# Performance work log

Measured on AMD Instinct MI355X. Metric: run time of the kernel, lower is better.

Reference implementation:

```python
import jax, jax.numpy as jnp
import numpy as np

BS, V, S, K = 4, 2048, 7, 10
CLASS_NUM, VEC_NUM, CAT = 6, 8, 16
OUT_HEAD = CLASS_NUM + VEC_NUM * 3  # 30
DIM_FUSE = 128 + 128 + 256 + 256 + 512 + 512 + 16  # 1808


def _normalize(x, axis):
    return x / jnp.maximum(jnp.linalg.norm(x, axis=axis, keepdims=True), 1e-12)


def knn_index(verts, k):
    # verts: (b, v, 3) -> (b, v, k) excluding self
    inner = jnp.einsum('bnd,bmd->bnm', verts, verts)
    sq = jnp.sum(verts * verts, axis=2)
    dist = sq[:, :, None] + sq[:, None, :] - 2.0 * inner
    _, idx = jax.lax.top_k(-dist, k + 1)
    return idx[:, :, 1:]


def nearest_index(target, source):
    # target: (b, v1, 3), source: (b, v2, 3) -> (b, v1)
    inner = jnp.einsum('bnd,bmd->bnm', target, source)
    d = jnp.sum(source * source, 2)[:, None, :] + jnp.sum(target * target, 2)[:, :, None] - 2.0 * inner
    return jnp.argmin(d, axis=-1)


def gather_nb(t, idx):
    # t: (b, v, d), idx: (b, v1, k) -> (b, v1, k, d)
    return jax.vmap(lambda tt, ii: tt[ii])(t, idx)


def gather1(t, idx):
    # t: (b, v, d), idx: (b, v1) -> (b, v1, d)
    return jax.vmap(lambda tt, ii: tt[ii])(t, idx)


def bn_train(x, g, b, eps=1e-5):
    # x: (b, v, c); BatchNorm1d training-mode over (batch, vertices)
    m = jnp.mean(x, axis=(0, 1), keepdims=True)
    v = jnp.var(x, axis=(0, 1), keepdims=True)
    return (x - m) * jax.lax.rsqrt(v + eps) * g + b


def conv_surface(nb_idx, verts, directions, s, kernel_num):
    nd = _normalize(gather_nb(verts, nb_idx) - verts[:, :, None, :], -1)  # (b,v,n,3)
    sd = _normalize(directions, 0)  # (3, s*k)
    theta = jax.nn.relu(jnp.einsum('bvnd,dk->bvnk', nd, sd))
    b_, v_, n_, _ = theta.shape
    theta = theta.reshape(b_, v_, n_, s, kernel_num)
    return jnp.sum(jnp.max(theta, axis=2), axis=2)  # (b, v, kernel_num)


def conv_layer(nb_idx, verts, fm, w, b, directions, s, out_ch):
    nd = _normalize(gather_nb(verts, nb_idx) - verts[:, :, None, :], -1)
    sd = _normalize(directions, 0)  # (3, s*out_ch)
    theta = jax.nn.relu(jnp.einsum('bvnd,dk->bvnk', nd, sd))  # (b,v,n,s*o)
    fo = jnp.einsum('bvc,ck->bvk', fm, w) + b  # (b, v, (s+1)*o)
    center = fo[..., :out_ch]
    supp = gather_nb(fo[..., out_ch:], nb_idx)  # (b,v,n,s*o)
    act = (theta * supp).reshape(theta.shape[0], theta.shape[1], theta.shape[2], s, out_ch)
    act = jnp.sum(jnp.max(act, axis=2), axis=2)  # (b, v, o)
    return center + act


def pool_layer(verts, fm, pooling_rate, nb_num):
    idx = knn_index(verts, nb_num)
    pooled = jnp.max(gather_nb(fm, idx), axis=2)
    pool_num = verts.shape[1] // pooling_rate
    # deterministic subsample (torch uses randperm; fixed arange for reproducibility)
    return verts[:, :pool_num], pooled[:, :pool_num]


def setup_inputs() -> dict:
    key = jax.random.key(0)
    ks = jax.random.split(key, 16)
    def rn(i, shape, scale=0.05):
        return jax.random.normal(ks[i], shape, dtype=jnp.float32) * scale
    z = lambda *s: jnp.zeros(s, jnp.float32)
    o = lambda *s: jnp.ones(s, jnp.float32)
    return {
        'vertices': jax.random.normal(ks[0], (BS, V, 3), dtype=jnp.float32),
        'onehot': jax.nn.one_hot(jax.random.randint(ks[1], (BS,), 0, CAT), CAT, dtype=jnp.float32),
        'dir0': rn(2, (3, S * 128)),
        'w1': rn(3, (128, (S + 1) * 128)), 'b1': z((S + 1) * 128), 'dir1': rn(4, (3, S * 128)),
        'w2': rn(5, (128, (S + 1) * 256)), 'b2': z((S + 1) * 256), 'dir2': rn(6, (3, S * 256)),
        'w3': rn(7, (256, (S + 1) * 256)), 'b3': z((S + 1) * 256), 'dir3': rn(8, (3, S * 256)),
        'w4': rn(9, (256, (S + 1) * 512)), 'b4': z((S + 1) * 512), 'dir4': rn(10, (3, S * 512)),
        'g_bn1': o(128), 'be_bn1': z(128),
        'g_bn2': o(256), 'be_bn2': z(256),
        'g_bn3': o(256), 'be_bn3': z(256),
        'wc1': rn(11, (512, DIM_FUSE)), 'bc1': z(512),
        'wc2': rn(12, (512, 512)), 'bc2': z(512),
        'wc3': rn(13, (OUT_HEAD, 512)), 'bc3': z(OUT_HEAD),
    }


def reference(vertices, onehot, dir0, w1, b1, dir1, w2, b2, dir2, w3, b3, dir3,
              w4, b4, dir4, g_bn1, be_bn1, g_bn2, be_bn2, g_bn3, be_bn3,
              wc1, bc1, wc2, bc2, wc3, bc3):
    bs, v_num, _ = vertices.shape
    nb = knn_index(vertices, K)
    fm0 = jax.nn.relu(conv_surface(nb, vertices, dir0, S, 128))
    fm1 = jax.nn.relu(bn_train(conv_layer(nb, vertices, fm0, w1, b1, dir1, S, 128), g_bn1, be_bn1))
    vp1, fp1 = pool_layer(vertices, fm1, 4, 4)
    nb1 = knn_index(vp1, min(K, vp1.shape[1] // 8))
    fm2 = jax.nn.relu(bn_train(conv_layer(nb1, vp1, fp1, w2, b2, dir2, S, 256), g_bn2, be_bn2))
    fm3 = jax.nn.relu(bn_train(conv_layer(nb1, vp1, fm2, w3, b3, dir3, S, 256), g_bn3, be_bn3))
    vp2, fp2 = pool_layer(vp1, fm3, 4, 4)
    nb2 = knn_index(vp2, min(K, vp2.shape[1] // 8))
    fm4 = conv_layer(nb2, vp2, fp2, w4, b4, dir4, S, 512)
    f_global = jnp.max(fm4, axis=1)  # (b, 512)
    n1 = nearest_index(vertices, vp1)
    n2 = nearest_index(vertices, vp2)
    fm2u = gather1(fm2, n1)
    fm3u = gather1(fm3, n1)
    fm4u = gather1(fm4, n2)
    fg = jnp.broadcast_to(f_global[:, None, :], (bs, v_num, 512))
    oh = jnp.broadcast_to(onehot[:, None, :], (bs, v_num, CAT))
    feat = jnp.concatenate([fm0, fm1, fm2u, fm3u, fm4u, oh], axis=2)
    fuse = jnp.concatenate([fm0, fm1, fm2u, fm3u, fm4u, fg, oh], axis=2)
    h = jax.nn.relu(jnp.einsum('bvc,oc->bvo', fuse, wc1) + bc1)
    h = jax.nn.relu(jnp.einsum('bvc,oc->bvo', h, wc2) + bc2)
    pred = jnp.einsum('bvc,oc->bvo', h, wc3) + bc3
    seg = pred[..., :CLASS_NUM]
    vecs = pred[..., CLASS_NUM:CLASS_NUM + VEC_NUM * 3]
    return (seg, vecs, feat)
```

## Files before the change

### kernel.cpp

```cpp
#include <hip/hip_runtime.h>
#include <hip/hip_bf16.h>
#include <math.h>

#define BSZ 4
#define VN 2048
#define SS 7
#define KNB 10

typedef __attribute__((ext_vector_type(8))) short short8;
typedef __attribute__((ext_vector_type(4))) float f32x4;

__device__ inline ushort f2bf(float x) {
    __hip_bfloat16 h = __float2bfloat16(x);
    return *(ushort*)&h;
}

__device__ inline unsigned fenc(float f) {
    unsigned b = __float_as_uint(f);
    return (b & 0x80000000u) ? ~b : (b | 0x80000000u);
}
__device__ inline float fdec(unsigned e) {
    unsigned b = (e & 0x80000000u) ? (e & 0x7FFFFFFFu) : ~e;
    return __uint_as_float(b);
}

#define PB0 8960L
#define PB1 24320L
#define PB2 958208L
#define PB3 1220352L

__global__ void prep_uber(const float* __restrict__ d0, const float* __restrict__ d1,
                          const float* __restrict__ d2, const float* __restrict__ d3,
                          const float* __restrict__ d4,
                          float* __restrict__ s0, float* __restrict__ s1,
                          float* __restrict__ s2, float* __restrict__ s3, float* __restrict__ s4,
                          const float* __restrict__ wc3, float* __restrict__ wc3t,
                          const float* __restrict__ wc1, ushort* __restrict__ wc1b,
                          const float* __restrict__ wc2, ushort* __restrict__ wc2b) {
    long i = blockIdx.x * 256L + threadIdx.x;
    if (i < PB0) {
        const float* src; float* dst; int C, c;
        if (i < 896)        { src = d0; dst = s0; C = 896;  c = (int)i; }
        else if (i < 1792)  { src = d1; dst = s1; C = 896;  c = (int)i - 896; }
        else if (i < 3584)  { src = d2; dst = s2; C = 1792; c = (int)i - 1792; }
        else if (i < 5376)  { src = d3; dst = s3; C = 1792; c = (int)i - 3584; }
        else                { src = d4; dst = s4; C = 3584; c = (int)i - 5376; }
        float a = src[c], b = src[C + c], e = src[2 * C + c];
        float den = fmaxf(sqrtf(a * a + b * b + e * e), 1e-12f);
        dst[c] = a / den; dst[C + c] = b / den; dst[2 * C + c] = e / den;
    } else if (i < PB1) {
        long j = i - PB0;
        int o = (int)(j / 512), k = (int)(j % 512);
        wc3t[(long)k * 30 + o] = wc3[j];
    } else if (i < PB2) {
        long j = i - PB1;
        int c = (int)(j % 1824);
        long r = j / 1824;
        wc1b[j] = f2bf(c < 1808 ? wc1[r * 1808 + c] : 0.f);
    } else if (i < PB3) {
        long j = i - PB2;
        wc2b[j] = f2bf(wc2[j]);
    }
}

__global__ __launch_bounds__(256) void wt_trans_all(const float* __restrict__ w1, const float* __restrict__ w2,
                                                    const float* __restrict__ w3, const float* __restrict__ w4,
                                                    ushort* __restrict__ o1, ushort* __restrict__ o2,
                                                    ushort* __restrict__ o3, ushort* __restrict__ o4) {
    __shared__ float tile[32][33];
    int gb = blockIdx.x;
    const float* w; ushort* o; int K, N, t;
    if (gb < 128)      { w = w1; o = o1; K = 128; N = 1024; t = gb; }
    else if (gb < 384) { w = w2; o = o2; K = 128; N = 2048; t = gb - 128; }
    else if (gb < 896) { w = w3; o = o3; K = 256; N = 2048; t = gb - 384; }
    else               { w = w4; o = o4; K = 256; N = 4096; t = gb - 896; }
    int tn = t % (N / 32), tk = t / (N / 32);
    int n0 = tn * 32, k0 = tk * 32;
    int tx = threadIdx.x % 32, ty = threadIdx.x / 32;
#pragma unroll
    for (int r = 0; r < 32; r += 8)
        tile[ty + r][tx] = w[(long)(k0 + ty + r) * N + n0 + tx];
    __syncthreads();
#pragma unroll
    for (int r = 0; r < 32; r += 8)
        o[(long)(n0 + ty + r) * K + k0 + tx] = f2bf(tile[tx][ty + r]);
}

#define KOFF0 0L
#define KOFF1 1310720L
#define KOFF2 1392640L
#define KOFF3 1397760L
#define KOFF4 1528832L
#define KTOT  1537024L

template <int KK>
__device__ void knn_part_dev(const float* __restrict__ verts, int Nsrc, int T, int nch,
                             int tile, int b, int ch,
                             float* __restrict__ pd, int* __restrict__ pi,
                             float4* __restrict__ s4) {
    int len = Nsrc / nch;
    const float* vb = verts + (long)b * VN * 3;
    int j0 = ch * len;
    for (int j = threadIdx.x; j < len; j += 256) {
        float x = vb[(j0 + j) * 3 + 0];
        float y = vb[(j0 + j) * 3 + 1];
        float z = vb[(j0 + j) * 3 + 2];
        s4[j] = make_float4(x, y, z, x * x + y * y + z * z);
    }
    __syncthreads();
    int i = tile * 256 + threadIdx.x;
    if (i >= T) return;
    float px = vb[i * 3], py = vb[i * 3 + 1], pz = vb[i * 3 + 2];
    float d[KK]; int id[KK];
#pragma unroll
    for (int q = 0; q < KK; q++) { d[q] = 1e30f; id[q] = 0; }
    for (int j = 0; j < len; j++) {
        float4 s = s4[j];
        float dot = px * s.x + py * s.y + pz * s.z;
        float dd = fmaf(-2.f, dot, s.w);
        int jj = j0 + j;
        dd = (jj == i) ? 1e30f : dd;
        if (__any(dd < d[KK - 1])) {
#pragma unroll
            for (int q = 0; q < KK; q++) {
                bool lt = dd < d[q];
                float dmin = lt ? dd : d[q];
                float dmax = lt ? d[q] : dd;
                int imin = lt ? jj : id[q];
                int imax = lt ? id[q] : jj;
                d[q] = dmin; id[q] = imin; dd = dmax; jj = imax;
            }
        }
    }
    long base = (((long)b * T + i) * nch + ch) * KK;
#pragma unroll
    for (int q = 0; q < KK; q++) { pd[base + q] = d[q]; pi[base + q] = id[q]; }
}

__device__ void nearest_dev(const float* __restrict__ verts, int SN, int* __restrict__ out,
                            int gl, float4* __restrict__ s4) {
    int t = gl * 256 + threadIdx.x;
    int b = t / VN;
    const float* vb = verts + (long)b * VN * 3;
    for (int j = threadIdx.x; j < SN; j += 256) {
        float x = vb[j * 3], y = vb[j * 3 + 1], z = vb[j * 3 + 2];
        s4[j] = make_float4(x, y, z, x * x + y * y + z * z);
    }
    __syncthreads();
    int i = t % VN;
    float px = vb[i * 3], py = vb[i * 3 + 1], pz = vb[i * 3 + 2];
    float best = 1e30f; int bi = 0;
    for (int j = 0; j < SN; j++) {
        float4 s = s4[j];
        float dot = px * s.x + py * s.y + pz * s.z;
        float dd = fmaf(-2.f, dot, s.w);
        bool lt = dd < best;
        best = lt ? dd : best;
        bi = lt ? j : bi;
    }
    out[t] = bi;
}

__global__ __launch_bounds__(256) void knn_part_uber(const float* __restrict__ verts,
                                                     float* __restrict__ pd, int* __restrict__ pi,
                                                     int* __restrict__ n1, int* __restrict__ n2) {
    __shared__ float4 smem[512];
    int gb = blockIdx.x;
    if (gb < 512) {
        int tile = gb % 8, bc = gb / 8;
        knn_part_dev<10>(verts, 2048, 2048, 16, tile, bc / 16, bc % 16, pd + KOFF0, pi + KOFF0, smem);
    } else if (gb < 544) {
        int local = gb - 512, tile = local % 2, bc = local / 2;
        knn_part_dev<10>(verts, 512, 512, 4, tile, bc / 4, bc % 4, pd + KOFF1, pi + KOFF1, smem);
    } else if (gb < 548) {
        int bc = gb - 544;
        knn_part_dev<10>(verts, 128, 128, 1, 0, bc, 0, pd + KOFF2, pi + KOFF2, smem);
    } else if (gb < 676) {
        int local = gb - 548, tile = local % 2, bc = local / 2;
        knn_part_dev<4>(verts, 2048, 512, 16, tile, bc / 16, bc % 16, pd + KOFF3, pi + KOFF3, smem);
    } else if (gb < 692) {
        int bc = gb - 676;
        knn_part_dev<4>(verts, 512, 128, 4, 0, bc / 4, bc % 4, pd + KOFF4, pi + KOFF4, smem);
    } else if (gb < 724) {
        nearest_dev(verts, 512, n1, gb - 692, smem);
    } else {
        nearest_dev(verts, 128, n2, gb - 724, smem);
    }
}

template <int KK, int NCH>
__device__ void knn_merge_dev(const float* __restrict__ pd, const int* __restrict__ pi,
                              int t, int* __restrict__ out) {
    float d[KK]; int id[KK];
#pragma unroll
    for (int q = 0; q < KK; q++) { d[q] = 1e30f; id[q] = 0; }
    for (int c = 0; c < NCH; c++) {
        long base = ((long)t * NCH + c) * KK;
        for (int q = 0; q < KK; q++) {
            float dd = pd[base + q];
            if (dd >= d[KK - 1]) break;
            int jj = pi[base + q];
#pragma unroll
            for (int p = 0; p < KK; p++) {
                bool lt = dd < d[p];
                float dmin = lt ? dd : d[p];
                float dmax = lt ? d[p] : dd;
                int imin = lt ? jj : id[p];
                int imax = lt ? id[p] : jj;
                d[p] = dmin; id[p] = imin; dd = dmax; jj = imax;
            }
        }
    }
#pragma unroll
    for (int q = 0; q < KK; q++) out[(long)t * KK + q] = id[q];
}

__global__ void knn_merge_uber(const float* __restrict__ pd, const int* __restrict__ pi,
                               int* __restrict__ nb, int* __restrict__ nb1, int* __restrict__ nb2,
                               int* __restrict__ nbp1, int* __restrict__ nbp2) {
    int gt = blockIdx.x * 256 + threadIdx.x;
    if (gt < 8192)       knn_merge_dev<10, 16>(pd + KOFF0, pi + KOFF0, gt, nb);
    else if (gt < 10240) knn_merge_dev<10, 4>(pd + KOFF1, pi + KOFF1, gt - 8192, nb1);
    else if (gt < 10752) knn_merge_dev<10, 1>(pd + KOFF2, pi + KOFF2, gt - 10240, nb2);
    else if (gt < 12800) knn_merge_dev<4, 16>(pd + KOFF3, pi + KOFF3, gt - 10752, nbp1);
    else                 knn_merge_dev<4, 4>(pd + KOFF4, pi + KOFF4, gt - 12800, nbp2);
}

__global__ void conv_surface_kernel(const float* __restrict__ verts, const int* __restrict__ nb,
                                    const float* __restrict__ sd, float* __restrict__ fm0,
                                    ushort* __restrict__ fm0b) {
    int bv = blockIdx.x;
    int b = bv / VN, v = bv % VN;
    __shared__ float snd[KNB][3];
    int tid = threadIdx.x;
    if (tid < KNB) {
        int nj = nb[(long)bv * KNB + tid];
        const float* vb = verts + (long)b * VN * 3;
        float dx = vb[nj * 3] - vb[v * 3];
        float dy = vb[nj * 3 + 1] - vb[v * 3 + 1];
        float dz = vb[nj * 3 + 2] - vb[v * 3 + 2];
        float den = fmaxf(sqrtf(dx * dx + dy * dy + dz * dz), 1e-12f);
        snd[tid][0] = dx / den; snd[tid][1] = dy / den; snd[tid][2] = dz / den;
    }
    __syncthreads();
    int c = tid;
    float acc = 0.f;
    for (int s = 0; s < SS; s++) {
        int col = s * 128 + c;
        float s0 = sd[col], s1 = sd[896 + col], s2 = sd[2 * 896 + col];
        float m = 0.f;
#pragma unroll
        for (int n = 0; n < KNB; n++) {
            float dot = snd[n][0] * s0 + snd[n][1] * s1 + snd[n][2] * s2;
            m = fmaxf(m, dot);
        }
        acc += m;
    }
    fm0[(long)bv * 128 + c] = acc;
    fm0b[(long)bv * 128 + c] = f2bf(acc);
}

__global__ void conv_act_kernel(const float* __restrict__ verts, const int* __restrict__ nb,
                                const float* __restrict__ sd, const float* __restrict__ fo,
                                float* __restrict__ out, unsigned* __restrict__ fgmax,
                                int Vl, int outC) {
    int bv = blockIdx.x;
    int b = bv / Vl, v = bv % Vl;
    __shared__ float snd[KNB][3];
    __shared__ int srow[KNB];
    int tid = threadIdx.x;
    if (tid < KNB) {
        int nj = nb[(long)bv * KNB + tid];
        srow[tid] = b * Vl + nj;
        const float* vb = verts + (long)b * VN * 3;
        float dx = vb[nj * 3] - vb[v * 3];
        float dy = vb[nj * 3 + 1] - vb[v * 3 + 1];
        float dz = vb[nj * 3 + 2] - vb[v * 3 + 2];
        float den = fmaxf(sqrtf(dx * dx + dy * dy + dz * dz), 1e-12f);
        snd[tid][0] = dx / den; snd[tid][1] = dy / den; snd[tid][2] = dz / den;
    }
    __syncthreads();
    int c = tid;
    int SC = SS * outC;
    int foN = SC + outC;
    float acc = fo[(long)bv * foN + c];
    for (int s = 0; s < SS; s++) {
        int col = s * outC + c;
        float s0 = sd[col], s1 = sd[SC + col], s2 = sd[2 * SC + col];
        float m = -1e30f;
#pragma unroll
        for (int n = 0; n < KNB; n++) {
            float dot = snd[n][0] * s0 + snd[n][1] * s1 + snd[n][2] * s2;
            float th = fmaxf(dot, 0.f);
            float sup = fo[(long)srow[n] * foN + outC + col];
            m = fmaxf(m, th * sup);
        }
        acc += m;
    }
    out[(long)bv * outC + c] = acc;
    if (fgmax) atomicMax(&fgmax[b * outC + c], fenc(acc));
}

__global__ __launch_bounds__(256) void bn_stat_kernel(const float* __restrict__ x,
                                                      float* __restrict__ stat, int R, int C) {
    int rp = 256 / C;
    int c = threadIdx.x % C;
    int rs = threadIdx.x / C;
    float s = 0.f, s2 = 0.f;
    for (long r = (long)blockIdx.x * rp + rs; r < R; r += (long)gridDim.x * rp) {
        float v = x[r * C + c];
        s += v; s2 += v * v;
    }
    atomicAdd(&stat[c], s);
    atomicAdd(&stat[C + c], s2);
}

__global__ void bn_apply_relu_kernel(const float* __restrict__ x, const float* __restrict__ stat,
                                     const float* __restrict__ g, const float* __restrict__ be,
                                     float* __restrict__ out, ushort* __restrict__ outb, int R, int C) {
    long i = blockIdx.x * 256L + threadIdx.x;
    if (i >= (long)R * C) return;
    int c = (int)(i % C);
    float mu = stat[c] / R;
    float var = stat[C + c] / R - mu * mu;
    var = fmaxf(var, 0.f);
    float y = (x[i] - mu) * rsqrtf(var + 1e-5f) * g[c] + be[c];
    y = fmaxf(y, 0.f);
    out[i] = y;
    if (outb) outb[i] = f2bf(y);
}

__global__ void pool_b_kernel(const float* __restrict__ fm, const int* __restrict__ idx,
                              ushort* __restrict__ out, int Vin, int T, int C) {
    long i = blockIdx.x * 256L + threadIdx.x;
    if (i >= (long)BSZ * T * C) return;
    int c = (int)(i % C);
    long bt = i / C;
    int b = (int)(bt / T), t = (int)(bt % T);
    const int* id = idx + ((long)b * T + t) * 4;
    float m = -1e30f;
#pragma unroll
    for (int n = 0; n < 4; n++)
        m = fmaxf(m, fm[((long)b * Vin + id[n]) * C + c]);
    out[i] = f2bf(m);
}

__global__ __launch_bounds__(256) void gemm_mfma_bt_kernel(
    const ushort* __restrict__ A, const ushort* __restrict__ Bt,
    const float* __restrict__ bias, float* __restrict__ Cf, ushort* __restrict__ Cb,
    int M, int N, int K, int relu)
{
    __shared__ ushort As[128 * 32];
    __shared__ ushort Bs[128 * 32];
    int t = threadIdx.x;
    int w = t >> 6, l = t & 63;
    int quad = l >> 4, lm = l & 15;
    int wm = w >> 1, wn = w & 1;
    long m0 = blockIdx.y * 128L;
    long n0 = blockIdx.x * 128L;
    int lr = t >> 2;
    int lk = (t & 3) * 8;
    f32x4 acc[4][4];
#pragma unroll
    for (int i = 0; i < 4; i++)
#pragma unroll
        for (int j = 0; j < 4; j++) acc[i][j] = (f32x4){0.f, 0.f, 0.f, 0.f};

    for (int k0 = 0; k0 < K; k0 += 32) {
        uint4 a0 = *(const uint4*)(A + (m0 + lr) * K + k0 + lk);
        uint4 a1 = *(const uint4*)(A + (m0 + 64 + lr) * K + k0 + lk);
        uint4 b0 = *(const uint4*)(Bt + (n0 + lr) * K + k0 + lk);
        uint4 b1 = *(const uint4*)(Bt + (n0 + 64 + lr) * K + k0 + lk);
        __syncthreads();
        *(uint4*)&As[lr * 32 + lk] = a0;
        *(uint4*)&As[(64 + lr) * 32 + lk] = a1;
        *(uint4*)&Bs[lr * 32 + lk] = b0;
        *(uint4*)&Bs[(64 + lr) * 32 + lk] = b1;
        __syncthreads();
        short8 af[4], bfr[4];
#pragma unroll
        for (int i = 0; i < 4; i++)
            af[i] = *(const short8*)&As[(wm * 64 + i * 16 + lm) * 32 + quad * 8];
#pragma unroll
        for (int j = 0; j < 4; j++)
            bfr[j] = *(const short8*)&Bs[(wn * 64 + j * 16 + lm) * 32 + quad * 8];
#pragma unroll
        for (int i = 0; i < 4; i++)
#pragma unroll
            for (int j = 0; j < 4; j++)
                acc[i][j] = __builtin_amdgcn_mfma_f32_16x16x32_bf16(af[i], bfr[j], acc[i][j], 0, 0, 0);
    }
#pragma unroll
    for (int i = 0; i < 4; i++) {
#pragma unroll
        for (int j = 0; j < 4; j++) {
            int n = (int)n0 + wn * 64 + j * 16 + lm;
            float bv = bias[n];
#pragma unroll
            for (int r = 0; r < 4; r++) {
                int m = (int)m0 + wm * 64 + i * 16 + quad * 4 + r;
                float v = acc[i][j][r] + bv;
                if (relu) v = fmaxf(v, 0.f);
                if (Cf) Cf[(long)m * N + n] = v;
                if (Cb) Cb[(long)m * N + n] = f2bf(v);
            }
        }
    }
}

__global__ __launch_bounds__(256) void gemm_mfma_bt64_kernel(
    const ushort* __restrict__ A, const ushort* __restrict__ Bt,
    const float* __restrict__ bias, float* __restrict__ Cf, ushort* __restrict__ Cb,
    int M, int N, int K, int relu)
{
    __shared__ ushort As[64 * 32];
    __shared__ ushort Bs[128 * 32];
    int t = threadIdx.x;
    int w = t >> 6, l = t & 63;
    int quad = l >> 4, lm = l & 15;
    int wm = w >> 1, wn = w & 1;
    long m0 = blockIdx.y * 64L;
    long n0 = blockIdx.x * 128L;
    int lr = t >> 2;
    int lk = (t & 3) * 8;
    f32x4 acc[2][4];
#pragma unroll
    for (int i = 0; i < 2; i++)
#pragma unroll
        for (int j = 0; j < 4; j++) acc[i][j] = (f32x4){0.f, 0.f, 0.f, 0.f};

    for (int k0 = 0; k0 < K; k0 += 32) {
        uint4 a0 = *(const uint4*)(A + (m0 + lr) * K + k0 + lk);
        uint4 b0 = *(const uint4*)(Bt + (n0 + lr) * K + k0 + lk);
        uint4 b1 = *(const uint4*)(Bt + (n0 + 64 + lr) * K + k0 + lk);
        __syncthreads();
        *(uint4*)&As[lr * 32 + lk] = a0;
        *(uint4*)&Bs[lr * 32 + lk] = b0;
        *(uint4*)&Bs[(64 + lr) * 32 + lk] = b1;
        __syncthreads();
        short8 af[2], bfr[4];
#pragma unroll
        for (int i = 0; i < 2; i++)
            af[i] = *(const short8*)&As[(wm * 32 + i * 16 + lm) * 32 + quad * 8];
#pragma unroll
        for (int j = 0; j < 4; j++)
            bfr[j] = *(const short8*)&Bs[(wn * 64 + j * 16 + lm) * 32 + quad * 8];
#pragma unroll
        for (int i = 0; i < 2; i++)
#pragma unroll
            for (int j = 0; j < 4; j++)
                acc[i][j] = __builtin_amdgcn_mfma_f32_16x16x32_bf16(af[i], bfr[j], acc[i][j], 0, 0, 0);
    }
#pragma unroll
    for (int i = 0; i < 2; i++) {
#pragma unroll
        for (int j = 0; j < 4; j++) {
            int n = (int)n0 + wn * 64 + j * 16 + lm;
            float bv = bias[n];
#pragma unroll
            for (int r = 0; r < 4; r++) {
                int m = (int)m0 + wm * 32 + i * 16 + quad * 4 + r;
                float v = acc[i][j][r] + bv;
                if (relu) v = fmaxf(v, 0.f);
                if (Cf) Cf[(long)m * N + n] = v;
                if (Cb) Cb[(long)m * N + n] = f2bf(v);
            }
        }
    }
}

__global__ __launch_bounds__(256) void wc3_kernel(const float* __restrict__ h2,
                                                  const float* __restrict__ wc3t,
                                                  const float* __restrict__ bc3,
                                                  float* __restrict__ out) {
    int r8 = threadIdx.x >> 5;
    int c = threadIdx.x & 31;
    long row = blockIdx.x * 8L + r8;
    const float* hr = h2 + row * 512;
    float acc = 0.f;
    if (c < 30) {
        for (int k = 0; k < 512; k++)
            acc += hr[k] * wc3t[k * 30 + c];
        acc += bc3[c];
        if (c < 6) out[row * 6 + c] = acc;
        else       out[49152 + row * 24 + (c - 6)] = acc;
    }
}

__global__ void fuse_bf_kernel(const float* __restrict__ fm0, const float* __restrict__ fm1,
                               const float* __restrict__ fm2, const float* __restrict__ fm3,
                               const float* __restrict__ fm4, const unsigned* __restrict__ fg_enc,
                               const float* __restrict__ onehot,
                               const int* __restrict__ n1, const int* __restrict__ n2,
                               ushort* __restrict__ fuse_b, float* __restrict__ feat) {
    long i = blockIdx.x * 256L + threadIdx.x;
    if (i >= 8192L * 1824) return;
    int c = (int)(i % 1824);
    long row = i / 1824;
    int b = (int)(row / VN);
    float val = 0.f;
    if (c < 128)       val = fm0[row * 128 + c];
    else if (c < 256)  val = fm1[row * 128 + (c - 128)];
    else if (c < 512)  val = fm2[((long)b * 512 + n1[row]) * 256 + (c - 256)];
    else if (c < 768)  val = fm3[((long)b * 512 + n1[row]) * 256 + (c - 512)];
    else if (c < 1280) val = fm4[((long)b * 128 + n2[row]) * 512 + (c - 768)];
    else if (c < 1792) val = fdec(fg_enc[b * 512 + (c - 1280)]);
    else if (c < 1808) val = onehot[b * 16 + (c - 1792)];
    fuse_b[i] = f2bf(val);
    if (c < 1280)                   feat[row * 1296 + c] = val;
    else if (c >= 1792 && c < 1808) feat[row * 1296 + (c - 512)] = val;
}


extern "C" void kernel_launch(void* const* d_in, const int* in_sizes, int n_in,
                              void* d_out, int out_size, void* d_ws, size_t ws_size,
                              hipStream_t stream) {
    const float* verts  = (const float*)d_in[0];
    const float* onehot = (const float*)d_in[1];
    const float* dir0 = (const float*)d_in[2];
    const float* w1 = (const float*)d_in[3];
    const float* b1 = (const float*)d_in[4];
    const float* dir1 = (const float*)d_in[5];
    const float* w2 = (const float*)d_in[6];
    const float* b2 = (const float*)d_in[7];
    const float* dir2 = (const float*)d_in[8];
    const float* w3 = (const float*)d_in[9];
    const float* b3 = (const float*)d_in[10];
    const float* dir3 = (const float*)d_in[11];
    const float* w4 = (const float*)d_in[12];
    const float* b4 = (const float*)d_in[13];
    const float* dir4 = (const float*)d_in[14];
    const float* g_bn1 = (const float*)d_in[15];
    const float* be_bn1 = (const float*)d_in[16];
    const float* g_bn2 = (const float*)d_in[17];
    const float* be_bn2 = (const float*)d_in[18];
    const float* g_bn3 = (const float*)d_in[19];
    const float* be_bn3 = (const float*)d_in[20];
    const float* wc1 = (const float*)d_in[21];
    const float* bc1 = (const float*)d_in[22];
    const float* wc2 = (const float*)d_in[23];
    const float* bc2 = (const float*)d_in[24];
    const float* wc3 = (const float*)d_in[25];
    const float* bc3 = (const float*)d_in[26];
    float* outf = (float*)d_out;

    float* wsf = (float*)d_ws;
    size_t off = 0;
    auto alloc = [&](size_t n) { float* p = wsf + off; off += (n + 15) & ~(size_t)15; return p; };

    float* sd0 = alloc(3 * 896);
    float* sd1 = alloc(3 * 896);
    float* sd2 = alloc(3 * 1792);
    float* sd3 = alloc(3 * 1792);
    float* sd4 = alloc(3 * 3584);
    float* wc3t = alloc(512L * 30);
    float* fm0 = alloc(8192L * 128);
    float* fm1 = alloc(8192L * 128);
    float* c1  = alloc(8192L * 128);
    float* fm2 = alloc(2048L * 256);
    float* c2  = alloc(2048L * 256);
    float* fm3 = alloc(2048L * 256);
    float* c3  = alloc(2048L * 256);
    float* fm4 = alloc(512L * 512);
    float* statbase = alloc(3328);
    float* stat1 = statbase;
    float* stat2 = statbase + 256;
    float* stat3 = statbase + 768;
    unsigned* fg_enc = (unsigned*)(statbase + 1280);
    float* fbuf = alloc(8192L * 1024);
    float* h2 = alloc(8192L * 512);
    float* pd  = alloc(KTOT);
    int* pi    = (int*)alloc(KTOT);
    int* nb   = (int*)alloc(8192L * KNB);
    int* nb1  = (int*)alloc(2048L * KNB);
    int* nb2  = (int*)alloc(512L * KNB);
    int* nbp1 = (int*)alloc(2048L * 4);
    int* nbp2 = (int*)alloc(512L * 4);
    int* n1   = (int*)alloc(8192);
    int* n2   = (int*)alloc(8192);
    ushort* fuse_b = (ushort*)alloc(8192L * 1824 / 2);
    ushort* h1b    = (ushort*)alloc(8192L * 512 / 2);
    ushort* wc1b   = (ushort*)alloc(512L * 1824 / 2);
    ushort* wc2b   = (ushort*)alloc(512L * 512 / 2);
    ushort* w1tb   = (ushort*)alloc(1024L * 128 / 2);
    ushort* w2tb   = (ushort*)alloc(2048L * 128 / 2);
    ushort* w3tb   = (ushort*)alloc(2048L * 256 / 2);
    ushort* w4tb   = (ushort*)alloc(4096L * 256 / 2);
    ushort* fm0b   = (ushort*)alloc(8192L * 128 / 2);
    ushort* fp1b   = (ushort*)alloc(2048L * 128 / 2);
    ushort* fm2b   = (ushort*)alloc(2048L * 256 / 2);
    ushort* fp2b   = (ushort*)alloc(512L * 256 / 2);

    auto nblk = [](long n, int b) { return (unsigned)((n + b - 1) / b); };

    hipMemsetAsync(statbase, 0, 3328 * sizeof(float), stream);
    prep_uber<<<nblk(PB3, 256), 256, 0, stream>>>(dir0, dir1, dir2, dir3, dir4,
                                                  sd0, sd1, sd2, sd3, sd4,
                                                  wc3, wc3t, wc1, wc1b, wc2, wc2b);
    wt_trans_all<<<1920, 256, 0, stream>>>(w1, w2, w3, w4, w1tb, w2tb, w3tb, w4tb);

    knn_part_uber<<<756, 256, 0, stream>>>(verts, pd, pi, n1, n2);
    knn_merge_uber<<<52, 256, 0, stream>>>(pd, pi, nb, nb1, nb2, nbp1, nbp2);

    conv_surface_kernel<<<BSZ * 2048, 128, 0, stream>>>(verts, nb, sd0, fm0, fm0b);

    gemm_mfma_bt_kernel<<<dim3(8, 64), 256, 0, stream>>>(fm0b, w1tb, b1, fbuf, nullptr, 8192, 1024, 128, 0);
    conv_act_kernel<<<BSZ * 2048, 128, 0, stream>>>(verts, nb, sd1, fbuf, c1, nullptr, 2048, 128);
    bn_stat_kernel<<<256, 256, 0, stream>>>(c1, stat1, 8192, 128);
    bn_apply_relu_kernel<<<nblk(8192L * 128, 256), 256, 0, stream>>>(c1, stat1, g_bn1, be_bn1, fm1, nullptr, 8192, 128);

    pool_b_kernel<<<nblk(BSZ * 512L * 128, 256), 256, 0, stream>>>(fm1, nbp1, fp1b, 2048, 512, 128);

    gemm_mfma_bt64_kernel<<<dim3(16, 32), 256, 0, stream>>>(fp1b, w2tb, b2, fbuf, nullptr, 2048, 2048, 128, 0);
    conv_act_kernel<<<BSZ * 512, 256, 0, stream>>>(verts, nb1, sd2, fbuf, c2, nullptr, 512, 256);
    bn_stat_kernel<<<256, 256, 0, stream>>>(c2, stat2, 2048, 256);
    bn_apply_relu_kernel<<<nblk(2048L * 256, 256), 256, 0, stream>>>(c2, stat2, g_bn2, be_bn2, fm2, fm2b, 2048, 256);

    gemm_mfma_bt64_kernel<<<dim3(16, 32), 256, 0, stream>>>(fm2b, w3tb, b3, fbuf, nullptr, 2048, 2048, 256, 0);
    conv_act_kernel<<<BSZ * 512, 256, 0, stream>>>(verts, nb1, sd3, fbuf, c3, nullptr, 512, 256);
    bn_stat_kernel<<<256, 256, 0, stream>>>(c3, stat3, 2048, 256);
    bn_apply_relu_kernel<<<nblk(2048L * 256, 256), 256, 0, stream>>>(c3, stat3, g_bn3, be_bn3, fm3, nullptr, 2048, 256);

    pool_b_kernel<<<nblk(BSZ * 128L * 256, 256), 256, 0, stream>>>(fm3, nbp2, fp2b, 512, 128, 256);

    gemm_mfma_bt64_kernel<<<dim3(32, 8), 256, 0, stream>>>(fp2b, w4tb, b4, fbuf, nullptr, 512, 4096, 256, 0);
    conv_act_kernel<<<BSZ * 128, 512, 0, stream>>>(verts, nb2, sd4, fbuf, fm4, fg_enc, 128, 512);

    fuse_bf_kernel<<<nblk(8192L * 1824, 256), 256, 0, stream>>>(fm0, fm1, fm2, fm3, fm4, fg_enc, onehot,
                                                                n1, n2, fuse_b, outf + 245760);

    gemm_mfma_bt64_kernel<<<dim3(4, 128), 256, 0, stream>>>(fuse_b, wc1b, bc1, nullptr, h1b, 8192, 512, 1824, 1);
    gemm_mfma_bt64_kernel<<<dim3(4, 128), 256, 0, stream>>>(h1b, wc2b, bc2, h2, nullptr, 8192, 512, 512, 1);
    wc3_kernel<<<1024, 256, 0, stream>>>(h2, wc3t, bc3, outf);
}
```

Measured before the change: 505.1 us.

## Split kNN scans into dual top-k lists, use direct global-to-LDS loads, row-wise fuse

The kNN partial kernel now keeps two independent top-k insertion lists per thread over two halves of a fixed 128-point chunk, with no wave-level early exit. This gives more instruction-level parallelism at the cost of doubling the partial results the merge stage reads. The nearest-neighbour search likewise runs two independent argmin chains. The MFMA GEMMs replace register-staged global loads with global_load_lds, moving tiles straight into LDS, and the fuse kernel is restructured to one block per row so the gather indices are loaded once per row. The chunk length is hardcoded to 128, which silently assumes the existing chunk counts.

Result: no change. 510.4 us (+1.1%).

```diff
diff --git a/kernel.cpp b/kernel.cpp
--- a/kernel.cpp
+++ b/kernel.cpp
@@ -9,12 +9,18 @@
 
 typedef __attribute__((ext_vector_type(8))) short short8;
 typedef __attribute__((ext_vector_type(4))) float f32x4;
+typedef __attribute__((address_space(1))) const void gcvoid;
+typedef __attribute__((address_space(3))) void lvoid;
 
 __device__ inline ushort f2bf(float x) {
     __hip_bfloat16 h = __float2bfloat16(x);
     return *(ushort*)&h;
 }
 
+__device__ inline void gl2lds16(const ushort* g, ushort* l) {
+    __builtin_amdgcn_global_load_lds((gcvoid*)g, (lvoid*)l, 16, 0, 0);
+}
+
 __device__ inline unsigned fenc(float f) {
     unsigned b = __float_as_uint(f);
     return (b & 0x80000000u) ? ~b : (b | 0x80000000u);
@@ -23,6 +29,11 @@
     unsigned b = (e & 0x80000000u) ? (e & 0x7FFFFFFFu) : ~e;
     return __uint_as_float(b);
 }
+
+#define INS(dq, iq, dd, jj) { bool lt_ = (dd) < (dq); \
+    float dmn_ = lt_ ? (dd) : (dq); float dmx_ = lt_ ? (dq) : (dd); \
+    int imn_ = lt_ ? (jj) : (iq); int imx_ = lt_ ? (iq) : (jj); \
+    (dq) = dmn_; (iq) = imn_; (dd) = dmx_; (jj) = imx_; }
 
 #define PB0 8960L
 #define PB1 24320L
@@ -87,21 +98,20 @@
 }
 
 #define KOFF0 0L
-#define KOFF1 1310720L
-#define KOFF2 1392640L
-#define KOFF3 1397760L
-#define KOFF4 1528832L
-#define KTOT  1537024L
+#define KOFF1 2621440L
+#define KOFF2 2785280L
+#define KOFF3 2795520L
+#define KOFF4 3057664L
+#define KTOT  3074048L
 
 template <int KK>
 __device__ void knn_part_dev(const float* __restrict__ verts, int Nsrc, int T, int nch,
                              int tile, int b, int ch,
                              float* __restrict__ pd, int* __restrict__ pi,
                              float4* __restrict__ s4) {
-    int len = Nsrc / nch;
     const float* vb = verts + (long)b * VN * 3;
-    int j0 = ch * len;
-    for (int j = threadIdx.x; j < len; j += 256) {
+    int j0 = ch * 128;
+    for (int j = threadIdx.x; j < 128; j += 256) {
         float x = vb[(j0 + j) * 3 + 0];
         float y = vb[(j0 + j) * 3 + 1];
         float z = vb[(j0 + j) * 3 + 2];
@@ -111,30 +121,27 @@
     int i = tile * 256 + threadIdx.x;
     if (i >= T) return;
     float px = vb[i * 3], py = vb[i * 3 + 1], pz = vb[i * 3 + 2];
-    float d[KK]; int id[KK];
-#pragma unroll
-    for (int q = 0; q < KK; q++) { d[q] = 1e30f; id[q] = 0; }
-    for (int j = 0; j < len; j++) {
-        float4 s = s4[j];
-        float dot = px * s.x + py * s.y + pz * s.z;
-        float dd = fmaf(-2.f, dot, s.w);
-        int jj = j0 + j;
-        dd = (jj == i) ? 1e30f : dd;
-        if (__any(dd < d[KK - 1])) {
-#pragma unroll
-            for (int q = 0; q < KK; q++) {
-                bool lt = dd < d[q];
-                float dmin = lt ? dd : d[q];
-                float dmax = lt ? d[q] : dd;
-                int imin = lt ? jj : id[q];
-                int imax = lt ? id[q] : jj;
-                d[q] = dmin; id[q] = imin; dd = dmax; jj = imax;
-            }
-        }
-    }
-    long base = (((long)b * T + i) * nch + ch) * KK;
-#pragma unroll
-    for (int q = 0; q < KK; q++) { pd[base + q] = d[q]; pi[base + q] = id[q]; }
+    float d0[KK], d1[KK]; int id0[KK], id1[KK];
+#pragma unroll
+    for (int q = 0; q < KK; q++) { d0[q] = 1e30f; id0[q] = 0; d1[q] = 1e30f; id1[q] = 0; }
+    for (int j = 0; j < 64; j++) {
+        float4 sA = s4[j];
+        float4 sB = s4[64 + j];
+        float dA = fmaf(-2.f, px * sA.x + py * sA.y + pz * sA.z, sA.w);
+        float dB = fmaf(-2.f, px * sB.x + py * sB.y + pz * sB.z, sB.w);
+        int jA = j0 + j, jB = j0 + 64 + j;
+        dA = (jA == i) ? 1e30f : dA;
+        dB = (jB == i) ? 1e30f : dB;
+#pragma unroll
+        for (int q = 0; q < KK; q++) { INS(d0[q], id0[q], dA, jA); }
+#pragma unroll
+        for (int q = 0; q < KK; q++) { INS(d1[q], id1[q], dB, jB); }
+    }
+    long base = (((long)b * T + i) * nch * 2 + 2 * ch) * KK;
+#pragma unroll
+    for (int q = 0; q < KK; q++) { pd[base + q] = d0[q]; pi[base + q] = id0[q]; }
+#pragma unroll
+    for (int q = 0; q < KK; q++) { pd[base + KK + q] = d1[q]; pi[base + KK + q] = id1[q]; }
 }
 
 __device__ void nearest_dev(const float* __restrict__ verts, int SN, int* __restrict__ out,
@@ -149,16 +156,17 @@
     __syncthreads();
     int i = t % VN;
     float px = vb[i * 3], py = vb[i * 3 + 1], pz = vb[i * 3 + 2];
-    float best = 1e30f; int bi = 0;
-    for (int j = 0; j < SN; j++) {
-        float4 s = s4[j];
-        float dot = px * s.x + py * s.y + pz * s.z;
-        float dd = fmaf(-2.f, dot, s.w);
-        bool lt = dd < best;
-        best = lt ? dd : best;
-        bi = lt ? j : bi;
-    }
-    out[t] = bi;
+    int h = SN / 2;
+    float b0 = 1e30f, b1 = 1e30f; int i0 = 0, i1 = 0;
+    for (int j = 0; j < h; j++) {
+        float4 sA = s4[j];
+        float4 sB = s4[h + j];
+        float dA = fmaf(-2.f, px * sA.x + py * sA.y + pz * sA.z, sA.w);
+        float dB = fmaf(-2.f, px * sB.x + py * sB.y + pz * sB.z, sB.w);
+        bool lA = dA < b0; b0 = lA ? dA : b0; i0 = lA ? j : i0;
+        bool lB = dB < b1; b1 = lB ? dB : b1; i1 = lB ? (h + j) : i1;
+    }
+    out[t] = (b1 < b0) ? i1 : i0;
 }
 
 __global__ __launch_bounds__(256) void knn_part_uber(const float* __restrict__ verts,
@@ -201,14 +209,7 @@
             if (dd >= d[KK - 1]) break;
             int jj = pi[base + q];
 #pragma unroll
-            for (int p = 0; p < KK; p++) {
-                bool lt = dd < d[p];
-                float dmin = lt ? dd : d[p];
-                float dmax = lt ? d[p] : dd;
-                int imin = lt ? jj : id[p];
-                int imax = lt ? id[p] : jj;
-                d[p] = dmin; id[p] = imin; dd = dmax; jj = imax;
-            }
+            for (int p = 0; p < KK; p++) { INS(d[p], id[p], dd, jj); }
         }
     }
 #pragma unroll
@@ -219,11 +220,11 @@
                                int* __restrict__ nb, int* __restrict__ nb1, int* __restrict__ nb2,
                                int* __restrict__ nbp1, int* __restrict__ nbp2) {
     int gt = blockIdx.x * 256 + threadIdx.x;
-    if (gt < 8192)       knn_merge_dev<10, 16>(pd + KOFF0, pi + KOFF0, gt, nb);
-    else if (gt < 10240) knn_merge_dev<10, 4>(pd + KOFF1, pi + KOFF1, gt - 8192, nb1);
-    else if (gt < 10752) knn_merge_dev<10, 1>(pd + KOFF2, pi + KOFF2, gt - 10240, nb2);
-    else if (gt < 12800) knn_merge_dev<4, 16>(pd + KOFF3, pi + KOFF3, gt - 10752, nbp1);
-    else                 knn_merge_dev<4, 4>(pd + KOFF4, pi + KOFF4, gt - 12800, nbp2);
+    if (gt < 8192)       knn_merge_dev<10, 32>(pd + KOFF0, pi + KOFF0, gt, nb);
+    else if (gt < 10240) knn_merge_dev<10, 8>(pd + KOFF1, pi + KOFF1, gt - 8192, nb1);
+    else if (gt < 10752) knn_merge_dev<10, 2>(pd + KOFF2, pi + KOFF2, gt - 10240, nb2);
+    else if (gt < 12800) knn_merge_dev<4, 32>(pd + KOFF3, pi + KOFF3, gt - 10752, nbp1);
+    else                 knn_merge_dev<4, 8>(pd + KOFF4, pi + KOFF4, gt - 12800, nbp2);
 }
 
 __global__ void conv_surface_kernel(const float* __restrict__ verts, const int* __restrict__ nb,
@@ -367,15 +368,11 @@
         for (int j = 0; j < 4; j++) acc[i][j] = (f32x4){0.f, 0.f, 0.f, 0.f};
 
     for (int k0 = 0; k0 < K; k0 += 32) {
-        uint4 a0 = *(const uint4*)(A + (m0 + lr) * K + k0 + lk);
-        uint4 a1 = *(const uint4*)(A + (m0 + 64 + lr) * K + k0 + lk);
-        uint4 b0 = *(const uint4*)(Bt + (n0 + lr) * K + k0 + lk);
-        uint4 b1 = *(const uint4*)(Bt + (n0 + 64 + lr) * K + k0 + lk);
         __syncthreads();
-        *(uint4*)&As[lr * 32 + lk] = a0;
-        *(uint4*)&As[(64 + lr) * 32 + lk] = a1;
-        *(uint4*)&Bs[lr * 32 + lk] = b0;
-        *(uint4*)&Bs[(64 + lr) * 32 + lk] = b1;
+        gl2lds16(A + (m0 + lr) * K + k0 + lk, &As[lr * 32 + lk]);
+        gl2lds16(A + (m0 + 64 + lr) * K + k0 + lk, &As[(64 + lr) * 32 + lk]);
+        gl2lds16(Bt + (n0 + lr) * K + k0 + lk, &Bs[lr * 32 + lk]);
+        gl2lds16(Bt + (n0 + 64 + lr) * K + k0 + lk, &Bs[(64 + lr) * 32 + lk]);
         __syncthreads();
         short8 af[4], bfr[4];
 #pragma unroll
@@ -430,13 +427,10 @@
         for (int j = 0; j < 4; j++) acc[i][j] = (f32x4){0.f, 0.f, 0.f, 0.f};
 
     for (int k0 = 0; k0 < K; k0 += 32) {
-        uint4 a0 = *(const uint4*)(A + (m0 + lr) * K + k0 + lk);
-        uint4 b0 = *(const uint4*)(Bt + (n0 + lr) * K + k0 + lk);
-        uint4 b1 = *(const uint4*)(Bt + (n0 + 64 + lr) * K + k0 + lk);
         __syncthreads();
-        *(uint4*)&As[lr * 32 + lk] = a0;
-        *(uint4*)&Bs[lr * 32 + lk] = b0;
-        *(uint4*)&Bs[(64 + lr) * 32 + lk] = b1;
+        gl2lds16(A + (m0 + lr) * K + k0 + lk, &As[lr * 32 + lk]);
+        gl2lds16(Bt + (n0 + lr) * K + k0 + lk, &Bs[lr * 32 + lk]);
+        gl2lds16(Bt + (n0 + 64 + lr) * K + k0 + lk, &Bs[(64 + lr) * 32 + lk]);
         __syncthreads();
         short8 af[2], bfr[4];
 #pragma unroll
@@ -487,28 +481,41 @@
     }
 }
 
-__global__ void fuse_bf_kernel(const float* __restrict__ fm0, const float* __restrict__ fm1,
-                               const float* __restrict__ fm2, const float* __restrict__ fm3,
-                               const float* __restrict__ fm4, const unsigned* __restrict__ fg_enc,
-                               const float* __restrict__ onehot,
-                               const int* __restrict__ n1, const int* __restrict__ n2,
-                               ushort* __restrict__ fuse_b, float* __restrict__ feat) {
-    long i = blockIdx.x * 256L + threadIdx.x;
-    if (i >= 8192L * 1824) return;
-    int c = (int)(i % 1824);
-    long row = i / 1824;
-    int b = (int)(row / VN);
-    float val = 0.f;
-    if (c < 128)       val = fm0[row * 128 + c];
-    else if (c < 256)  val = fm1[row * 128 + (c - 128)];
-    else if (c < 512)  val = fm2[((long)b * 512 + n1[row]) * 256 + (c - 256)];
-    else if (c < 768)  val = fm3[((long)b * 512 + n1[row]) * 256 + (c - 512)];
-    else if (c < 1280) val = fm4[((long)b * 128 + n2[row]) * 512 + (c - 768)];
-    else if (c < 1792) val = fdec(fg_enc[b * 512 + (c - 1280)]);
-    else if (c < 1808) val = onehot[b * 16 + (c - 1792)];
-    fuse_b[i] = f2bf(val);
-    if (c < 1280)                   feat[row * 1296 + c] = val;
-    else if (c >= 1792 && c < 1808) feat[row * 1296 + (c - 512)] = val;
+__global__ __launch_bounds__(256) void fuse_bf_kernel(
+    const float* __restrict__ fm0, const float* __restrict__ fm1,
+    const float* __restrict__ fm2, const float* __restrict__ fm3,
+    const float* __restrict__ fm4, const unsigned* __restrict__ fg_enc,
+    const float* __restrict__ onehot,
+    const int* __restrict__ n1, const int* __restrict__ n2,
+    ushort* __restrict__ fuse_b, float* __restrict__ feat) {
+    long row = blockIdx.x;
+    int b = (int)(row >> 11);
+    int i1 = n1[row], i2 = n2[row];
+    const float* p0 = fm0 + row * 128;
+    const float* p1 = fm1 + row * 128;
+    const float* p2 = fm2 + ((long)b * 512 + i1) * 256;
+    const float* p3 = fm3 + ((long)b * 512 + i1) * 256;
+    const float* p4 = fm4 + ((long)b * 128 + i2) * 512;
+    const unsigned* pg = fg_enc + b * 512;
+    const float* po = onehot + b * 16;
+    ushort* fb = fuse_b + row * 1824;
+    float* ft = feat + row * 1296;
+#pragma unroll
+    for (int k = 0; k < 8; k++) {
+        int c = threadIdx.x + k * 256;
+        if (c >= 1824) break;
+        float val = 0.f;
+        if (c < 128)       val = p0[c];
+        else if (c < 256)  val = p1[c - 128];
+        else if (c < 512)  val = p2[c - 256];
+        else if (c < 768)  val = p3[c - 512];
+        else if (c < 1280) val = p4[c - 768];
+        else if (c < 1792) val = fdec(pg[c - 1280]);
+        else if (c < 1808) val = po[c - 1792];
+        fb[c] = f2bf(val);
+        if (c < 1280)                   ft[c] = val;
+        else if (c >= 1792 && c < 1808) ft[c - 512] = val;
+    }
 }
 
 
@@ -626,8 +633,8 @@
     gemm_mfma_bt64_kernel<<<dim3(32, 8), 256, 0, stream>>>(fp2b, w4tb, b4, fbuf, nullptr, 512, 4096, 256, 0);
     conv_act_kernel<<<BSZ * 128, 512, 0, stream>>>(verts, nb2, sd4, fbuf, fm4, fg_enc, 128, 512);
 
-    fuse_bf_kernel<<<nblk(8192L * 1824, 256), 256, 0, stream>>>(fm0, fm1, fm2, fm3, fm4, fg_enc, onehot,
-                                                                n1, n2, fuse_b, outf + 245760);
+    fuse_bf_kernel<<<8192, 256, 0, stream>>>(fm0, fm1, fm2, fm3, fm4, fg_enc, onehot,
+                                             n1, n2, fuse_b, outf + 245760);
 
     gemm_mfma_bt64_kernel<<<dim3(4, 128), 256, 0, stream>>>(fuse_b, wc1b, bc1, nullptr, h1b, 8192, 512, 1824, 1);
     gemm_mfma_bt64_kernel<<<dim3(4, 128), 256, 0, stream>>>(h1b, wc2b, bc2, h2, nullptr, 8192, 512, 512, 1);
```
